# Kernel tuning notes

Measured on AMD Instinct MI355X. Metric: run time of the kernel, lower is better.

Reference implementation:

```python
import jax, jax.numpy as jnp
import numpy as np

N = 100000
E = 1600000
DIMS = [64, 64, 64, 32]  # input -> hidden -> hidden -> num_classes
NEG_SLOPE = 0.01  # F.leaky_relu default


def setup_inputs() -> dict:
    key = jax.random.key(0)
    ks = jax.random.split(key, 8)
    inp = {
        "x": jax.random.normal(ks[0], (N, DIMS[0]), dtype=jnp.float32),
        "edge_index": jax.random.randint(ks[1], (2, E), 0, N, dtype=jnp.int64),
    }
    # GCNConv linear weights (glorot-ish scale) and biases
    for i in range(3):
        d_in, d_out = DIMS[i], DIMS[i + 1]
        scale = (2.0 / (d_in + d_out)) ** 0.5
        inp[f"W{i+1}"] = jax.random.normal(ks[2 + i], (d_in, d_out), dtype=jnp.float32) * scale
        inp[f"b{i+1}"] = jnp.zeros((d_out,), dtype=jnp.float32)
    return inp


def _gcn_conv(x, src, dst, norm, W, b):
    # x' = D^-1/2 (A+I) D^-1/2 (x W) + b
    h = x @ W                                   # [N, d_out]
    msg = h[src] * norm[:, None]                # gather + edge scaling  [E+N, d_out]
    out = jax.ops.segment_sum(msg, dst, num_segments=N)  # scatter-add
    return out + b


def reference(x, edge_index, W1, b1, W2, b2, W3, b3):
    loops = jnp.arange(N, dtype=edge_index.dtype)
    src = jnp.concatenate([edge_index[0], loops])  # add self-loops
    dst = jnp.concatenate([edge_index[1], loops])
    deg = jax.ops.segment_sum(jnp.ones_like(src, dtype=x.dtype), dst, num_segments=N)
    deg_isqrt = jax.lax.rsqrt(deg)              # deg >= 1 due to self-loops
    norm = deg_isqrt[src] * deg_isqrt[dst]      # [E+N]

    embeddings = []
    h = x
    for i, (W, b) in enumerate([(W1, b1), (W2, b2), (W3, b3)]):
        h = _gcn_conv(h, src, dst, norm, W, b)
        if i < 2:
            h = jnp.where(h >= 0, h, NEG_SLOPE * h)  # leaky_relu
        embeddings.append(h)
    return tuple(embeddings)
```

## Files before the change

### kernel.cpp

```cpp
#include <hip/hip_runtime.h>


constexpr int N_NODES = 100000;
constexpr int N_EDGES = 1600000;
constexpr int E4 = N_EDGES / 4;
constexpr float NEG = 0.01f;

constexpr int BSHIFT = 8;
constexpr int BKT_NODES = 1 << BSHIFT;
constexpr int NBKT = (N_NODES + BKT_NODES - 1) >> BSHIFT;
constexpr int EPB = 4096;
constexpr int ABLK = (N_EDGES + EPB - 1) / EPB;

constexpr int NTILES = N_NODES / 16;

using short8 = __attribute__((ext_vector_type(8))) short;
using float4v = __attribute__((ext_vector_type(4))) float;

__device__ __forceinline__ unsigned short f2bf(float f) {
    unsigned u = __float_as_uint(f);
    unsigned r = (u + 0x7fffu + ((u >> 16) & 1u)) >> 16;
    return (unsigned short)r;
}
__device__ __forceinline__ float bf2f(unsigned short us) {
    return __uint_as_float(((unsigned)us) << 16);
}

__global__ void bucket_count_kernel(const int* __restrict__ dst, int* __restrict__ bkt_cnt) {
    __shared__ int sc[NBKT];
    for (int i = threadIdx.x; i < NBKT; i += 256) sc[i] = 0;
    __syncthreads();
    for (int k = 0; k < 4; ++k) {
        int idx4 = blockIdx.x * 1024 + k * 256 + threadIdx.x;
        if (idx4 < E4) {
            const int4 d = *reinterpret_cast<const int4*>(dst + idx4 * 4);
            atomicAdd(&sc[d.x >> BSHIFT], 1);
            atomicAdd(&sc[d.y >> BSHIFT], 1);
            atomicAdd(&sc[d.z >> BSHIFT], 1);
            atomicAdd(&sc[d.w >> BSHIFT], 1);
        }
    }
    __syncthreads();
    for (int i = threadIdx.x; i < NBKT; i += 256) {
        int c = sc[i];
        if (c) atomicAdd(&bkt_cnt[i], c);
    }
}

__global__ void bucket_scan_kernel(const int* __restrict__ bkt_cnt,
                                   int* __restrict__ bkt_base, int* __restrict__ bkt_cursor) {
    __shared__ int s[512];
    int v = (threadIdx.x < NBKT) ? bkt_cnt[threadIdx.x] : 0;
    s[threadIdx.x] = v;
    __syncthreads();
    for (int off = 1; off < 512; off <<= 1) {
        int t = (threadIdx.x >= off) ? s[threadIdx.x - off] : 0;
        __syncthreads();
        s[threadIdx.x] += t;
        __syncthreads();
    }
    if (threadIdx.x < NBKT) {
        int b = s[threadIdx.x] - v;
        bkt_base[threadIdx.x] = b;
        bkt_cursor[threadIdx.x] = b;
    }
    if (threadIdx.x == NBKT) bkt_base[NBKT] = N_EDGES;
}

__global__ void bin_kernel(const int* __restrict__ src, const int* __restrict__ dst,
                           int* __restrict__ bkt_cursor, int2* __restrict__ pairs) {
    __shared__ int scnt[NBKT];
    __shared__ int sbase[NBKT];
    __shared__ int soff[NBKT];
    for (int i = threadIdx.x; i < NBKT; i += 256) { scnt[i] = 0; soff[i] = 0; }
    __syncthreads();
    for (int k = 0; k < 4; ++k) {
        int idx4 = blockIdx.x * 1024 + k * 256 + threadIdx.x;
        if (idx4 < E4) {
            const int4 d = *reinterpret_cast<const int4*>(dst + idx4 * 4);
            atomicAdd(&scnt[d.x >> BSHIFT], 1);
            atomicAdd(&scnt[d.y >> BSHIFT], 1);
            atomicAdd(&scnt[d.z >> BSHIFT], 1);
            atomicAdd(&scnt[d.w >> BSHIFT], 1);
        }
    }
    __syncthreads();
    for (int i = threadIdx.x; i < NBKT; i += 256) {
        int c = scnt[i];
        if (c) sbase[i] = atomicAdd(&bkt_cursor[i], c);
    }
    __syncthreads();
    for (int k = 0; k < 4; ++k) {
        int idx4 = blockIdx.x * 1024 + k * 256 + threadIdx.x;
        if (idx4 < E4) {
            const int4 s = *reinterpret_cast<const int4*>(src + idx4 * 4);
            const int4 d = *reinterpret_cast<const int4*>(dst + idx4 * 4);
            int b, pos;
            b = d.x >> BSHIFT; pos = sbase[b] + atomicAdd(&soff[b], 1); pairs[pos] = make_int2(s.x, d.x);
            b = d.y >> BSHIFT; pos = sbase[b] + atomicAdd(&soff[b], 1); pairs[pos] = make_int2(s.y, d.y);
            b = d.z >> BSHIFT; pos = sbase[b] + atomicAdd(&soff[b], 1); pairs[pos] = make_int2(s.z, d.z);
            b = d.w >> BSHIFT; pos = sbase[b] + atomicAdd(&soff[b], 1); pairs[pos] = make_int2(s.w, d.w);
        }
    }
}

__global__ void sort_pairs_kernel(const int2* __restrict__ pairs,
                                  const int* __restrict__ bkt_base,
                                  int2* __restrict__ pairs2) {
    __shared__ int s[512];
    __shared__ int sbase[NBKT];
    __shared__ int soff[NBKT];
    const int b = blockIdx.x;
    const int beg = bkt_base[b];
    const int end = bkt_base[b + 1];
    s[threadIdx.x] = 0;
    if (threadIdx.x < NBKT) soff[threadIdx.x] = 0;
    __syncthreads();
    for (int j = beg + threadIdx.x; j < end; j += 512) {
        atomicAdd(&s[pairs[j].x >> BSHIFT], 1);
    }
    __syncthreads();
    int v = s[threadIdx.x];
    __syncthreads();
    for (int off = 1; off < 512; off <<= 1) {
        int t = (threadIdx.x >= off) ? s[threadIdx.x - off] : 0;
        __syncthreads();
        s[threadIdx.x] += t;
        __syncthreads();
    }
    if (threadIdx.x < NBKT) sbase[threadIdx.x] = s[threadIdx.x] - v;
    __syncthreads();
    for (int j = beg + threadIdx.x; j < end; j += 512) {
        int2 p = pairs[j];
        int sb = p.x >> BSHIFT;
        int pos = beg + sbase[sb] + atomicAdd(&soff[sb], 1);
        pairs2[pos] = p;
    }
}

__global__ void build_csr_kernel(const int2* __restrict__ pairs,
                                 const int* __restrict__ bkt_base,
                                 int* __restrict__ rowptr, float* __restrict__ disq,
                                 int* __restrict__ csr_src) {
    __shared__ int scnt[BKT_NODES];
    __shared__ int ssc[BKT_NODES];
    __shared__ int scur[BKT_NODES];
    const int b = blockIdx.x;
    const int n0 = b << BSHIFT;
    const int nb = min(BKT_NODES, N_NODES - n0);
    const int beg = bkt_base[b];
    const int end = bkt_base[b + 1];
    scnt[threadIdx.x] = 0;
    __syncthreads();
    for (int j = beg + threadIdx.x; j < end; j += 256) {
        atomicAdd(&scnt[pairs[j].y - n0], 1);
    }
    __syncthreads();
    int v = scnt[threadIdx.x];
    ssc[threadIdx.x] = v;
    __syncthreads();
    for (int off = 1; off < 256; off <<= 1) {
        int t = (threadIdx.x >= off) ? ssc[threadIdx.x - off] : 0;
        __syncthreads();
        ssc[threadIdx.x] += t;
        __syncthreads();
    }
    int excl = ssc[threadIdx.x] - v;
    scur[threadIdx.x] = beg + excl;
    if (threadIdx.x < nb) {
        rowptr[n0 + threadIdx.x] = beg + excl;
        disq[n0 + threadIdx.x] = rsqrtf(1.0f + (float)v);
    }
    if (b == NBKT - 1 && threadIdx.x == 0) rowptr[N_NODES] = N_EDGES;
    __syncthreads();
    for (int j = beg + threadIdx.x; j < end; j += 256) {
        int2 p = pairs[j];
        int pos = atomicAdd(&scur[p.y - n0], 1);
        csr_src[pos] = p.x;
    }
}

template <int D_OUT>
__global__ __launch_bounds__(256) void linear_mfma_kernel(const float* __restrict__ in,
                                                          const float* __restrict__ W,
                                                          unsigned short* __restrict__ h) {
    constexpr int NCT = D_OUT / 16;
    const int wave = threadIdx.x >> 6;
    const int lane = threadIdx.x & 63;
    const int lg = lane >> 4;
    const int lm = lane & 15;

    short8 Bhi[NCT][2], Blo[NCT][2];
#pragma unroll
    for (int ct = 0; ct < NCT; ++ct)
#pragma unroll
        for (int kk = 0; kk < 2; ++kk)
#pragma unroll
            for (int j = 0; j < 8; ++j) {
                float wv = W[(kk * 32 + lg * 8 + j) * D_OUT + ct * 16 + lm];
                unsigned short hi = f2bf(wv);
                unsigned short lo = f2bf(wv - bf2f(hi));
                Bhi[ct][kk][j] = (short)hi;
                Blo[ct][kk][j] = (short)lo;
            }

    const int slot = blockIdx.x * 4 + wave;
#pragma unroll 1
    for (int i = 0; i < 4; ++i) {
        int tile = slot + i * 1564;
        if (tile >= NTILES) break;
        int row = tile * 16 + lm;

        short8 Ahi[2], Alo[2];
#pragma unroll
        for (int kk = 0; kk < 2; ++kk) {
            const float4 v0 = *reinterpret_cast<const float4*>(in + (size_t)row * 64 + kk * 32 + lg * 8);
            const float4 v1 = *reinterpret_cast<const float4*>(in + (size_t)row * 64 + kk * 32 + lg * 8 + 4);
            float av[8] = {v0.x, v0.y, v0.z, v0.w, v1.x, v1.y, v1.z, v1.w};
#pragma unroll
            for (int j = 0; j < 8; ++j) {
                unsigned short hi = f2bf(av[j]);
                unsigned short lo = f2bf(av[j] - bf2f(hi));
                Ahi[kk][j] = (short)hi;
                Alo[kk][j] = (short)lo;
            }
        }

        float4v acc[NCT];
#pragma unroll
        for (int ct = 0; ct < NCT; ++ct) acc[ct] = (float4v){0.f, 0.f, 0.f, 0.f};

#pragma unroll
        for (int ct = 0; ct < NCT; ++ct)
#pragma unroll
            for (int kk = 0; kk < 2; ++kk) {
                acc[ct] = __builtin_amdgcn_mfma_f32_16x16x32_bf16(Ahi[kk], Bhi[ct][kk], acc[ct], 0, 0, 0);
                acc[ct] = __builtin_amdgcn_mfma_f32_16x16x32_bf16(Ahi[kk], Blo[ct][kk], acc[ct], 0, 0, 0);
                acc[ct] = __builtin_amdgcn_mfma_f32_16x16x32_bf16(Alo[kk], Bhi[ct][kk], acc[ct], 0, 0, 0);
            }

#pragma unroll
        for (int ct = 0; ct < NCT; ++ct)
#pragma unroll
            for (int r = 0; r < 4; ++r) {
                int orow = tile * 16 + lg * 4 + r;
                h[(size_t)orow * D_OUT + ct * 16 + lm] = f2bf(acc[ct][r]);
            }
    }
}

template <int D, bool RELU>
__global__ void gather_finish_kernel(const int* __restrict__ rowptr,
                                     const int* __restrict__ csr_src,
                                     const unsigned short* __restrict__ h,
                                     const float* __restrict__ disq,
                                     const float* __restrict__ b,
                                     float* __restrict__ out) {
    constexpr int TPN = D / 4;
    int t = blockIdx.x * blockDim.x + threadIdx.x;
    int node = t / TPN;
    if (node >= N_NODES) return;
    int part = t % TPN;
    int beg = rowptr[node];
    int end = rowptr[node + 1];
    float4 a0 = {0.f, 0.f, 0.f, 0.f};
    float4 a1 = {0.f, 0.f, 0.f, 0.f};
    int j = beg;
    for (; j + 1 < end; j += 2) {
        int s0 = csr_src[j];
        int s1 = csr_src[j + 1];
        float w0 = disq[s0];
        float w1 = disq[s1];
        const ushort4 u0 = *reinterpret_cast<const ushort4*>(h + (size_t)s0 * D + part * 4);
        const ushort4 u1 = *reinterpret_cast<const ushort4*>(h + (size_t)s1 * D + part * 4);
        a0.x = fmaf(bf2f(u0.x), w0, a0.x); a1.x = fmaf(bf2f(u1.x), w1, a1.x);
        a0.y = fmaf(bf2f(u0.y), w0, a0.y); a1.y = fmaf(bf2f(u1.y), w1, a1.y);
        a0.z = fmaf(bf2f(u0.z), w0, a0.z); a1.z = fmaf(bf2f(u1.z), w1, a1.z);
        a0.w = fmaf(bf2f(u0.w), w0, a0.w); a1.w = fmaf(bf2f(u1.w), w1, a1.w);
    }
    if (j < end) {
        int s0 = csr_src[j];
        float w0 = disq[s0];
        const ushort4 u0 = *reinterpret_cast<const ushort4*>(h + (size_t)s0 * D + part * 4);
        a0.x = fmaf(bf2f(u0.x), w0, a0.x);
        a0.y = fmaf(bf2f(u0.y), w0, a0.y);
        a0.z = fmaf(bf2f(u0.z), w0, a0.z);
        a0.w = fmaf(bf2f(u0.w), w0, a0.w);
    }
    float dn = disq[node];
    const ushort4 hu = *reinterpret_cast<const ushort4*>(h + (size_t)node * D + part * 4);
    const float4 bv = *reinterpret_cast<const float4*>(b + part * 4);
    float4 acc;
    acc.x = fmaf(a0.x + a1.x + dn * bf2f(hu.x), dn, bv.x);
    acc.y = fmaf(a0.y + a1.y + dn * bf2f(hu.y), dn, bv.y);
    acc.z = fmaf(a0.z + a1.z + dn * bf2f(hu.z), dn, bv.z);
    acc.w = fmaf(a0.w + a1.w + dn * bf2f(hu.w), dn, bv.w);
    if (RELU) {
        acc.x = (acc.x >= 0.f) ? acc.x : NEG * acc.x;
        acc.y = (acc.y >= 0.f) ? acc.y : NEG * acc.y;
        acc.z = (acc.z >= 0.f) ? acc.z : NEG * acc.z;
        acc.w = (acc.w >= 0.f) ? acc.w : NEG * acc.w;
    }
    *reinterpret_cast<float4*>(out + (size_t)node * D + part * 4) = acc;
}

extern "C" void kernel_launch(void* const* d_in, const int* in_sizes, int n_in,
                              void* d_out, int out_size, void* d_ws, size_t ws_size,
                              hipStream_t stream) {
    const float* x  = (const float*)d_in[0];
    const int* ei   = (const int*)d_in[1];
    const int* src  = ei;
    const int* dst  = ei + N_EDGES;
    const float* W1 = (const float*)d_in[2];
    const float* b1 = (const float*)d_in[3];
    const float* W2 = (const float*)d_in[4];
    const float* b2 = (const float*)d_in[5];
    const float* W3 = (const float*)d_in[6];
    const float* b3 = (const float*)d_in[7];

    float* out  = (float*)d_out;
    float* emb1 = out;
    float* emb2 = out + (size_t)N_NODES * 64;
    float* emb3 = out + (size_t)N_NODES * 128;

    char* ws = (char*)d_ws;
    int*   bkt_cnt    = (int*)ws;   ws += sizeof(int) * (NBKT + 1);
    int*   bkt_base   = (int*)ws;   ws += sizeof(int) * (NBKT + 1);
    int*   bkt_cursor = (int*)ws;   ws += sizeof(int) * (NBKT + 1);
    ws = (char*)(((size_t)ws + 255) & ~(size_t)255);
    float* disq       = (float*)ws; ws += sizeof(float) * N_NODES;
    int*   rowptr     = (int*)ws;   ws += sizeof(int) * (N_NODES + 1);
    ws = (char*)(((size_t)ws + 255) & ~(size_t)255);
    int2*  pairs      = (int2*)ws;  ws += sizeof(int2) * N_EDGES;
    int2*  pairs2     = (int2*)ws;  ws += sizeof(int2) * N_EDGES;
    int*   csr_src    = (int*)ws;   ws += sizeof(int) * N_EDGES;
    unsigned short* h = (unsigned short*)ws; ws += sizeof(unsigned short) * (size_t)N_NODES * 64;

    const int BLK = 256;
    const int gN16  = (N_NODES * 16 + BLK - 1) / BLK;
    const int gN8   = (N_NODES * 8  + BLK - 1) / BLK;
    const int gMFMA = 391;

    hipMemsetAsync(bkt_cnt, 0, sizeof(int) * (NBKT + 1), stream);
    bucket_count_kernel<<<ABLK, BLK, 0, stream>>>(dst, bkt_cnt);
    bucket_scan_kernel<<<1, 512, 0, stream>>>(bkt_cnt, bkt_base, bkt_cursor);
    bin_kernel<<<ABLK, BLK, 0, stream>>>(src, dst, bkt_cursor, pairs);
    sort_pairs_kernel<<<NBKT, 512, 0, stream>>>(pairs, bkt_base, pairs2);
    build_csr_kernel<<<NBKT, BLK, 0, stream>>>(pairs2, bkt_base, rowptr, disq, csr_src);

    linear_mfma_kernel<64><<<gMFMA, BLK, 0, stream>>>(x, W1, h);
    gather_finish_kernel<64, true><<<gN16, BLK, 0, stream>>>(rowptr, csr_src, h, disq, b1, emb1);

    linear_mfma_kernel<64><<<gMFMA, BLK, 0, stream>>>(emb1, W2, h);
    gather_finish_kernel<64, true><<<gN16, BLK, 0, stream>>>(rowptr, csr_src, h, disq, b2, emb2);

    linear_mfma_kernel<32><<<gMFMA, BLK, 0, stream>>>(emb2, W3, h);
    gather_finish_kernel<32, false><<<gN8, BLK, 0, stream>>>(rowptr, csr_src, h, disq, b3, emb3);
}
```

Baseline: 302.5 us.

## Prescale linear output by source degree norm and widen gather to 8 features

The linear MFMA kernel now multiplies each output row by its own inverse-sqrt degree before storing in bf16. The gather then drops the per-edge disq[src] load and FMA and just sums rows. Each thread now handles 8 features with 16-byte loads, and the edge loop is unrolled by 4 for more memory parallelism. The prescaled bf16 values round slightly differently, and there are half as many threads per node, so fewer loads are in flight per node.

```diff
diff --git a/kernel.cpp b/kernel.cpp
--- a/kernel.cpp
+++ b/kernel.cpp
@@ -15,6 +15,7 @@
 constexpr int NTILES = N_NODES / 16;
 
 using short8 = __attribute__((ext_vector_type(8))) short;
+using ushort8 = __attribute__((ext_vector_type(8))) unsigned short;
 using float4v = __attribute__((ext_vector_type(4))) float;
 
 __device__ __forceinline__ unsigned short f2bf(float f) {
@@ -183,6 +184,7 @@
 template <int D_OUT>
 __global__ __launch_bounds__(256) void linear_mfma_kernel(const float* __restrict__ in,
                                                           const float* __restrict__ W,
+                                                          const float* __restrict__ disq,
                                                           unsigned short* __restrict__ h) {
     constexpr int NCT = D_OUT / 16;
     const int wave = threadIdx.x >> 6;
@@ -240,68 +242,72 @@
             }
 
 #pragma unroll
-        for (int ct = 0; ct < NCT; ++ct)
-#pragma unroll
-            for (int r = 0; r < 4; ++r) {
-                int orow = tile * 16 + lg * 4 + r;
-                h[(size_t)orow * D_OUT + ct * 16 + lm] = f2bf(acc[ct][r]);
+        for (int r = 0; r < 4; ++r) {
+            int orow = tile * 16 + lg * 4 + r;
+            float dr = disq[orow];
+#pragma unroll
+            for (int ct = 0; ct < NCT; ++ct) {
+                h[(size_t)orow * D_OUT + ct * 16 + lm] = f2bf(acc[ct][r] * dr);
             }
+        }
     }
 }
 
 template <int D, bool RELU>
-__global__ void gather_finish_kernel(const int* __restrict__ rowptr,
+__global__ __launch_bounds__(256) void gather_finish_kernel(const int* __restrict__ rowptr,
                                      const int* __restrict__ csr_src,
                                      const unsigned short* __restrict__ h,
                                      const float* __restrict__ disq,
                                      const float* __restrict__ b,
                                      float* __restrict__ out) {
-    constexpr int TPN = D / 4;
+    constexpr int TPN = D / 8;
     int t = blockIdx.x * blockDim.x + threadIdx.x;
     int node = t / TPN;
     if (node >= N_NODES) return;
     int part = t % TPN;
+    const unsigned short* hp = h + part * 8;
     int beg = rowptr[node];
     int end = rowptr[node + 1];
-    float4 a0 = {0.f, 0.f, 0.f, 0.f};
-    float4 a1 = {0.f, 0.f, 0.f, 0.f};
+    float acc0[8], acc1[8];
+#pragma unroll
+    for (int k = 0; k < 8; ++k) { acc0[k] = 0.f; acc1[k] = 0.f; }
     int j = beg;
-    for (; j + 1 < end; j += 2) {
+    for (; j + 3 < end; j += 4) {
         int s0 = csr_src[j];
         int s1 = csr_src[j + 1];
-        float w0 = disq[s0];
-        float w1 = disq[s1];
-        const ushort4 u0 = *reinterpret_cast<const ushort4*>(h + (size_t)s0 * D + part * 4);
-        const ushort4 u1 = *reinterpret_cast<const ushort4*>(h + (size_t)s1 * D + part * 4);
-        a0.x = fmaf(bf2f(u0.x), w0, a0.x); a1.x = fmaf(bf2f(u1.x), w1, a1.x);
-        a0.y = fmaf(bf2f(u0.y), w0, a0.y); a1.y = fmaf(bf2f(u1.y), w1, a1.y);
-        a0.z = fmaf(bf2f(u0.z), w0, a0.z); a1.z = fmaf(bf2f(u1.z), w1, a1.z);
-        a0.w = fmaf(bf2f(u0.w), w0, a0.w); a1.w = fmaf(bf2f(u1.w), w1, a1.w);
-    }
-    if (j < end) {
+        int s2 = csr_src[j + 2];
+        int s3 = csr_src[j + 3];
+        const ushort8 u0 = *reinterpret_cast<const ushort8*>(hp + (size_t)s0 * D);
+        const ushort8 u1 = *reinterpret_cast<const ushort8*>(hp + (size_t)s1 * D);
+        const ushort8 u2 = *reinterpret_cast<const ushort8*>(hp + (size_t)s2 * D);
+        const ushort8 u3 = *reinterpret_cast<const ushort8*>(hp + (size_t)s3 * D);
+#pragma unroll
+        for (int k = 0; k < 8; ++k) {
+            acc0[k] += bf2f(u0[k]) + bf2f(u2[k]);
+            acc1[k] += bf2f(u1[k]) + bf2f(u3[k]);
+        }
+    }
+    for (; j < end; ++j) {
         int s0 = csr_src[j];
-        float w0 = disq[s0];
-        const ushort4 u0 = *reinterpret_cast<const ushort4*>(h + (size_t)s0 * D + part * 4);
-        a0.x = fmaf(bf2f(u0.x), w0, a0.x);
-        a0.y = fmaf(bf2f(u0.y), w0, a0.y);
-        a0.z = fmaf(bf2f(u0.z), w0, a0.z);
-        a0.w = fmaf(bf2f(u0.w), w0, a0.w);
+        const ushort8 u0 = *reinterpret_cast<const ushort8*>(hp + (size_t)s0 * D);
+#pragma unroll
+        for (int k = 0; k < 8; ++k) acc0[k] += bf2f(u0[k]);
     }
     float dn = disq[node];
-    const ushort4 hu = *reinterpret_cast<const ushort4*>(h + (size_t)node * D + part * 4);
-    const float4 bv = *reinterpret_cast<const float4*>(b + part * 4);
-    float4 acc;
-    acc.x = fmaf(a0.x + a1.x + dn * bf2f(hu.x), dn, bv.x);
-    acc.y = fmaf(a0.y + a1.y + dn * bf2f(hu.y), dn, bv.y);
-    acc.z = fmaf(a0.z + a1.z + dn * bf2f(hu.z), dn, bv.z);
-    acc.w = fmaf(a0.w + a1.w + dn * bf2f(hu.w), dn, bv.w);
-    if (RELU) {
-        acc.x = (acc.x >= 0.f) ? acc.x : NEG * acc.x;
-        acc.y = (acc.y >= 0.f) ? acc.y : NEG * acc.y;
-        acc.z = (acc.z >= 0.f) ? acc.z : NEG * acc.z;
-        acc.w = (acc.w >= 0.f) ? acc.w : NEG * acc.w;
-    }
-    *reinterpret_cast<float4*>(out + (size_t)node * D + part * 4) = acc;
+    const ushort8 un = *reinterpret_cast<const ushort8*>(hp + (size_t)node * D);
+    float res[8];
+#pragma unroll
+    for (int k = 0; k < 8; ++k) {
+        float bv = b[part * 8 + k];
+        float v = fmaf(acc0[k] + acc1[k] + bf2f(un[k]), dn, bv);
+        if (RELU) v = (v >= 0.f) ? v : NEG * v;
+        res[k] = v;
+    }
+    float4 lo = {res[0], res[1], res[2], res[3]};
+    float4 hi = {res[4], res[5], res[6], res[7]};
+    float* op = out + (size_t)node * D + part * 8;
+    *reinterpret_cast<float4*>(op) = lo;
+    *reinterpret_cast<float4*>(op + 4) = hi;
 }
 
 extern "C" void kernel_launch(void* const* d_in, const int* in_sizes, int n_in,
@@ -337,8 +343,8 @@
     unsigned short* h = (unsigned short*)ws; ws += sizeof(unsigned short) * (size_t)N_NODES * 64;
 
     const int BLK = 256;
-    const int gN16  = (N_NODES * 16 + BLK - 1) / BLK;
-    const int gN8   = (N_NODES * 8  + BLK - 1) / BLK;
+    const int gG64 = (N_NODES * 8 + BLK - 1) / BLK;
+    const int gG32 = (N_NODES * 4 + BLK - 1) / BLK;
     const int gMFMA = 391;
 
     hipMemsetAsync(bkt_cnt, 0, sizeof(int) * (NBKT + 1), stream);
@@ -348,12 +354,12 @@
     sort_pairs_kernel<<<NBKT, 512, 0, stream>>>(pairs, bkt_base, pairs2);
     build_csr_kernel<<<NBKT, BLK, 0, stream>>>(pairs2, bkt_base, rowptr, disq, csr_src);
 
-    linear_mfma_kernel<64><<<gMFMA, BLK, 0, stream>>>(x, W1, h);
-    gather_finish_kernel<64, true><<<gN16, BLK, 0, stream>>>(rowptr, csr_src, h, disq, b1, emb1);
-
-    linear_mfma_kernel<64><<<gMFMA, BLK, 0, stream>>>(emb1, W2, h);
-    gather_finish_kernel<64, true><<<gN16, BLK, 0, stream>>>(rowptr, csr_src, h, disq, b2, emb2);
-
-    linear_mfma_kernel<32><<<gMFMA, BLK, 0, stream>>>(emb2, W3, h);
-    gather_finish_kernel<32, false><<<gN8, BLK, 0, stream>>>(rowptr, csr_src, h, disq, b3, emb3);
-}
+    linear_mfma_kernel<64><<<gMFMA, BLK, 0, stream>>>(x, W1, disq, h);
+    gather_finish_kernel<64, true><<<gG64, BLK, 0, stream>>>(rowptr, csr_src, h, disq, b1, emb1);
+
+    linear_mfma_kernel<64><<<gMFMA, BLK, 0, stream>>>(emb1, W2, disq, h);
+    gather_finish_kernel<64, true><<<gG64, BLK, 0, stream>>>(rowptr, csr_src, h, disq, b2, emb2);
+
+    linear_mfma_kernel<32><<<gMFMA, BLK, 0, stream>>>(emb2, W3, disq, h);
+    gather_finish_kernel<32, false><<<gG32, BLK, 0, stream>>>(rowptr, csr_src, h, disq, b3, emb3);
+}
```

New measurement: 274.7 us. 1.1x faster.
